# Performance work log

Hardware: AMD Instinct MI355X
Metric: run time of the kernel (lower is better)

## Reference

```python
import jax, jax.numpy as jnp
import numpy as np

V, E, H, T = 30000, 512, 512, 32
B, L = 64, 512


def setup_inputs() -> dict:
    key = jax.random.key(0)
    ks = jax.random.split(key, 14)
    n = lambda k, shape: (jax.random.normal(k, shape, jnp.float32) * 0.05)
    return {
        "x": jax.random.randint(ks[0], (B, L), 0, V),
        "embedding": n(ks[1], (V, E)),
        # PyTorch LSTM params, gate order (i, f, g, o); biases b_ih+b_hh fused
        "w_ih_f": n(ks[2], (4 * H, E)),
        "w_hh_f": n(ks[3], (4 * H, H)),
        "b_f": n(ks[4], (4 * H,)),
        "w_ih_b": n(ks[5], (4 * H, E)),
        "w_hh_b": n(ks[6], (4 * H, H)),
        "b_b": n(ks[7], (4 * H,)),
        "W": n(ks[8], (T, 2 * H)),
        "b": n(ks[9], (T,)),
        # CRF params (torchcrf)
        "start": n(ks[10], (T,)),
        "end": n(ks[11], (T,)),
        "trans": n(ks[12], (T, T)),
    }


def _lstm(x, w_ih, w_hh, bias):
    # x: [L, B, E] -> hidden states [L, B, H]; PyTorch gate equations
    h_dim = w_hh.shape[1]
    xp = jnp.einsum('lbe,ge->lbg', x, w_ih) + bias  # precompute input proj [L,B,4H]

    def step(carry, xt):
        h, c = carry
        g = xt + h @ w_hh.T
        i, f, gg, o = jnp.split(g, 4, axis=-1)
        c = jax.nn.sigmoid(f) * c + jax.nn.sigmoid(i) * jnp.tanh(gg)
        h = jax.nn.sigmoid(o) * jnp.tanh(c)
        return (h, c), h

    bsz = x.shape[1]
    init = (jnp.zeros((bsz, h_dim), x.dtype), jnp.zeros((bsz, h_dim), x.dtype))
    _, hs = jax.lax.scan(step, init, xp)
    return hs


def _emissions(x, embedding, w_ih_f, w_hh_f, b_f, w_ih_b, w_hh_b, b_b, W, b):
    emb = embedding[x]                      # [B, L, E]
    xt = jnp.transpose(emb, (1, 0, 2))      # [L, B, E]
    hf = _lstm(xt, w_ih_f, w_hh_f, b_f)     # [L, B, H]
    hb = _lstm(xt[::-1], w_ih_b, w_hh_b, b_b)[::-1]
    h = jnp.concatenate([hf, hb], axis=-1)  # [L, B, 2H]
    return h @ W.T + b                      # [L, B, T]


def _viterbi(em, start, end, trans):
    # em: [L, B, T]; torchcrf CRF.decode with no mask (all timesteps valid)
    score = start + em[0]                   # [B, T]

    def step(score, em_t):
        nxt = score[:, :, None] + trans[None] + em_t[:, None, :]  # [B, T_prev, T_cur]
        return jnp.max(nxt, axis=1), jnp.argmax(nxt, axis=1)

    score, hist = jax.lax.scan(step, score, em[1:])  # hist: [L-1, B, T]
    score = score + end
    last = jnp.argmax(score, axis=-1)       # [B]

    def back(tag, idx_t):
        prev = jnp.take_along_axis(idx_t, tag[:, None], axis=1)[:, 0]
        return prev, prev

    _, prevs = jax.lax.scan(back, last, hist, reverse=True)  # [L-1, B]
    tags = jnp.concatenate([prevs, last[None]], axis=0)      # [L, B]
    return tags.T.astype(jnp.int32)                          # [B, L]


def reference(x, embedding, w_ih_f, w_hh_f, b_f, w_ih_b, w_hh_b, b_b, W, b, start, end, trans):
    em = _emissions(x, embedding, w_ih_f, w_hh_f, b_f, w_ih_b, w_hh_b, b_b, W, b)
    return _viterbi(em, start, end, trans)
```

## Files before the change

### kernel.cpp

```cpp
#include <hip/hip_runtime.h>
#include <cstdio>
#include <cstdint>


typedef float f32x4 __attribute__((ext_vector_type(4)));
typedef float f32x2 __attribute__((ext_vector_type(2)));

#define PKFMA(ACC, W2, H2) \
    asm("v_pk_fma_f32 %0, %1, %2, %0" : "+v"(ACC) : "v"(W2), "v"(H2))

__global__ __launch_bounds__(512) void k_gather(
    const int* __restrict__ x, const float* __restrict__ emb,
    float4* __restrict__ eg4)
{
    const int t   = blockIdx.x;
    const int tid = threadIdx.x;
    __shared__ int xv[64];
    if (tid < 64) xv[tid] = x[tid * 512 + t];
    __syncthreads();
    #pragma unroll
    for (int i = 0; i < 16; ++i) {
        const int flat = i * 512 + tid;
        const int b  = flat & 63;
        const int e4 = flat >> 6;
        const float4 v = *reinterpret_cast<const float4*>(
            emb + (size_t)xv[b] * 512 + e4 * 4);
        eg4[((size_t)t * 128 + e4) * 64 + b] = v;
    }
}

__global__ __launch_bounds__(256) void k_pack(
    const float* __restrict__ wih_f, const float* __restrict__ whh_f,
    const float* __restrict__ wih_b, const float* __restrict__ whh_b,
    float* __restrict__ wpack)
{
    const int i = blockIdx.x * 256 + threadIdx.x;
    const int j   = i & 3;
    const int r   = (i >> 2) & 7;
    const int kc  = (i >> 5) & 15;
    const int sec = (i >> 9) & 1;
    const int ks  = (i >> 10) & 7;
    const int wg  = (i >> 13) & 255;
    const int dir = (i >> 21) & 1;
    const int k   = ks * 64 + kc * 4 + j;
    const int g   = r >> 1, colL = r & 1;
    const int rg  = g * 512 + wg * 2 + colL;
    const float* wih = dir ? wih_b : wih_f;
    const float* whh = dir ? whh_b : whh_f;
    const float v = sec ? whh[(size_t)rg * 512 + k] : wih[(size_t)rg * 512 + k];
    wpack[i] = v;
}

__global__ __launch_bounds__(512, 2) void k_lstm(
    const float4* __restrict__ eg4, const float* __restrict__ wpack,
    const float* __restrict__ b_f, const float* __restrict__ b_b,
    float* __restrict__ h_f, float* __restrict__ h_b,
    int* __restrict__ bar)
{
    const int bid = blockIdx.x;
    const int dir = bid >> 8;
    const int wg  = bid & 255;
    float* HH       = dir ? h_b : h_f;
    const float* BS = dir ? b_b : b_f;
    int* ctr = bar + (size_t)dir * 65536;

    const int tid = threadIdx.x;
    const int b   = tid & 63;
    const int ks  = __builtin_amdgcn_readfirstlane(tid >> 6);

    __shared__ float wlds[8][1024];
    __shared__ float partb[8 * 8 * 64];
    __shared__ float hlds[64][2];

    {
        const float4* src = reinterpret_cast<const float4*>(
            wpack + (size_t)((dir * 256 + wg) * 8 + ks) * 1024);
        float4* dst = reinterpret_cast<float4*>(&wlds[ks][0]);
        #pragma unroll
        for (int i = 0; i < 4; ++i)
            dst[i * 64 + b] = src[i * 64 + b];
    }

    const int colL = (tid >> 6) & 1;
    float bias4[4] = {0.f, 0.f, 0.f, 0.f};
    if (tid < 128) {
        #pragma unroll
        for (int g = 0; g < 4; ++g) bias4[g] = BS[g * 512 + wg * 2 + colL];
    }
    float cst = 0.f;
    __syncthreads();

    const float* wl = &wlds[ks][0];

    f32x2 eacc2[8];
    #pragma unroll
    for (int r = 0; r < 8; ++r) eacc2[r] = (f32x2){0.f, 0.f};

    {
        const int t0 = dir ? 511 : 0;
        const float4* ep = eg4 + ((size_t)t0 * 128 + ks * 16) * 64 + b;
        #pragma unroll
        for (int half = 0; half < 2; ++half) {
            f32x4 v[8];
            #pragma unroll
            for (int kc = 0; kc < 8; ++kc)
                v[kc] = *reinterpret_cast<const f32x4*>(ep + (size_t)(half * 8 + kc) * 64);
            #pragma unroll
            for (int kc = 0; kc < 8; ++kc) {
                const float* wp = wl + (half * 8 + kc) * 32;
                const f32x2 elo = __builtin_shufflevector(v[kc], v[kc], 0, 1);
                const f32x2 ehi = __builtin_shufflevector(v[kc], v[kc], 2, 3);
                #pragma unroll
                for (int r = 0; r < 8; ++r) {
                    const f32x4 w4 = *reinterpret_cast<const f32x4*>(wp + r * 4);
                    const f32x2 wlo = __builtin_shufflevector(w4, w4, 0, 1);
                    const f32x2 whi = __builtin_shufflevector(w4, w4, 2, 3);
                    PKFMA(eacc2[r], wlo, elo);
                    PKFMA(eacc2[r], whi, ehi);
                }
            }
        }
    }

    for (int s = 0; s < 512; ++s) {
        const int t = dir ? (511 - s) : s;
        f32x2 acc2[8];
        #pragma unroll
        for (int r = 0; r < 8; ++r) acc2[r] = eacc2[r];

        if (s > 0) {
            const int* fp = ctr + ((size_t)(s - 1) * 8 + ks) * 16;
            while (__hip_atomic_load(fp, __ATOMIC_RELAXED,
                                     __HIP_MEMORY_SCOPE_AGENT) < 32)
                __builtin_amdgcn_s_sleep(1);

            const int tp = dir ? (t + 1) : (t - 1);
            const f32x2* hq = reinterpret_cast<const f32x2*>(HH)
                              + ((size_t)tp * 256 + ks * 32) * 64 + b;
            #pragma unroll
            for (int half = 0; half < 2; ++half) {
                f32x2 hv[16];
                #pragma unroll
                for (int kq = 0; kq < 16; ++kq)
                    hv[kq] = hq[(size_t)(half * 16 + kq) * 64];
                #pragma unroll
                for (int kc = 0; kc < 8; ++kc) {
                    const float* wp = wl + 512 + (half * 8 + kc) * 32;
                    #pragma unroll
                    for (int r = 0; r < 8; ++r) {
                        const f32x4 w4 = *reinterpret_cast<const f32x4*>(wp + r * 4);
                        const f32x2 wlo = __builtin_shufflevector(w4, w4, 0, 1);
                        const f32x2 whi = __builtin_shufflevector(w4, w4, 2, 3);
                        PKFMA(acc2[r], wlo, hv[kc * 2]);
                        PKFMA(acc2[r], whi, hv[kc * 2 + 1]);
                    }
                }
            }
        }

        #pragma unroll
        for (int r = 0; r < 8; ++r)
            partb[(ks * 8 + r) * 64 + b] = acc2[r][0] + acc2[r][1];
        __syncthreads();

        if (tid < 128) {
            float g4[4];
            #pragma unroll
            for (int g = 0; g < 4; ++g) {
                const int r = g * 2 + colL;
                float v = bias4[g];
                #pragma unroll
                for (int w = 0; w < 8; ++w) v += partb[(w * 8 + r) * 64 + b];
                g4[g] = v;
            }
            const float si = 1.f / (1.f + expf(-g4[0]));
            const float sf = 1.f / (1.f + expf(-g4[1]));
            const float tg = tanhf(g4[2]);
            const float so = 1.f / (1.f + expf(-g4[3]));
            cst = sf * cst + si * tg;
            hlds[b][colL] = so * tanhf(cst);
        }
        __syncthreads();

        if (tid < 64) {
            f32x2 o;
            o[0] = hlds[tid][0]; o[1] = hlds[tid][1];
            float* dst = HH + (((size_t)t * 256 + wg) * 64 + tid) * 2;
            asm volatile("global_store_dwordx2 %0, %1, off sc1"
                         :: "v"(dst), "v"(o) : "memory");
            asm volatile("s_waitcnt vmcnt(0)" ::: "memory");
            if (tid == 0 && s < 511)
                __hip_atomic_fetch_add(
                    ctr + ((size_t)s * 8 + (wg >> 5)) * 16, 1,
                    __ATOMIC_RELAXED, __HIP_MEMORY_SCOPE_AGENT);
        }

        if (s < 511) {
            const int tn = dir ? (t - 1) : (t + 1);
            const float4* ep = eg4 + ((size_t)tn * 128 + ks * 16) * 64 + b;
            #pragma unroll
            for (int r = 0; r < 8; ++r) eacc2[r] = (f32x2){0.f, 0.f};
            #pragma unroll
            for (int half = 0; half < 2; ++half) {
                f32x4 v[8];
                #pragma unroll
                for (int kc = 0; kc < 8; ++kc)
                    v[kc] = *reinterpret_cast<const f32x4*>(ep + (size_t)(half * 8 + kc) * 64);
                #pragma unroll
                for (int kc = 0; kc < 8; ++kc) {
                    const float* wp = wl + (half * 8 + kc) * 32;
                    const f32x2 elo = __builtin_shufflevector(v[kc], v[kc], 0, 1);
                    const f32x2 ehi = __builtin_shufflevector(v[kc], v[kc], 2, 3);
                    #pragma unroll
                    for (int r = 0; r < 8; ++r) {
                        const f32x4 w4 = *reinterpret_cast<const f32x4*>(wp + r * 4);
                        const f32x2 wlo = __builtin_shufflevector(w4, w4, 0, 1);
                        const f32x2 whi = __builtin_shufflevector(w4, w4, 2, 3);
                        PKFMA(eacc2[r], wlo, elo);
                        PKFMA(eacc2[r], whi, ehi);
                    }
                }
            }
        }
    }
}

__global__ __launch_bounds__(256) void k_em(
    const float* __restrict__ hf, const float* __restrict__ hb,
    const float* __restrict__ Wm, const float* __restrict__ bias,
    float* __restrict__ em)
{
    const int t   = blockIdx.x;
    const int tid = threadIdx.x;
    const int b   = tid & 63;
    const int tg  = tid >> 6;
    __shared__ float Wl[128][33];
    float acc[8] = {};

    for (int ch = 0; ch < 8; ++ch) {
        {
            const int tag = tid >> 3;
            const int kq  = tid & 7;
            const float* src = Wm + (size_t)tag * 1024 + ch * 128 + kq * 16;
            #pragma unroll
            for (int ii = 0; ii < 4; ++ii) {
                const float4 v = *reinterpret_cast<const float4*>(src + ii * 4);
                const int k0 = kq * 16 + ii * 4;
                Wl[k0 + 0][tag] = v.x; Wl[k0 + 1][tag] = v.y;
                Wl[k0 + 2][tag] = v.z; Wl[k0 + 3][tag] = v.w;
            }
        }
        __syncthreads();
        const f32x2* hsrc2 = (ch < 4)
            ? (reinterpret_cast<const f32x2*>(hf) + ((size_t)t * 256 + ch * 64) * 64 + b)
            : (reinterpret_cast<const f32x2*>(hb) + ((size_t)t * 256 + (ch - 4) * 64) * 64 + b);
        #pragma unroll 4
        for (int c2l = 0; c2l < 64; ++c2l) {
            const f32x2 h2 = hsrc2[(size_t)c2l * 64];
            #pragma unroll
            for (int j = 0; j < 2; ++j)
                #pragma unroll
                for (int jt = 0; jt < 8; ++jt)
                    acc[jt] = fmaf(h2[j], Wl[c2l * 2 + j][tg * 8 + jt], acc[jt]);
        }
        __syncthreads();
    }

    #pragma unroll
    for (int jt = 0; jt < 8; ++jt) {
        const int tag = tg * 8 + jt;
        em[((size_t)t * 64 + b) * 32 + tag] = acc[jt] + bias[tag];
    }
}

__global__ __launch_bounds__(64) void k_vit(
    const float* __restrict__ em, const float* __restrict__ startv,
    const float* __restrict__ endv, const float* __restrict__ trans,
    int* __restrict__ out)
{
    const int b    = blockIdx.x;
    const int lane = threadIdx.x;
    const int c    = lane & 31;
    const bool act = lane < 32;
    __shared__ unsigned char hist[511][32];
    __shared__ int outb[512];

    float tr[32];
    #pragma unroll 8
    for (int p = 0; p < 32; ++p) tr[p] = trans[p * 32 + c];

    float s = act ? (startv[c] + em[(size_t)b * 32 + c]) : -1e30f;

    for (int t = 1; t < 512; ++t) {
        const float emc = act ? em[((size_t)t * 64 + b) * 32 + c] : 0.f;
        float m = -1e30f; int arg = 0;
        #pragma unroll 8
        for (int p = 0; p < 32; ++p) {
            const float v = __shfl(s, p) + tr[p] + emc;
            if (v > m) { m = v; arg = p; }
        }
        if (act) { s = m; hist[t - 1][c] = (unsigned char)arg; }
    }

    s = act ? (s + endv[c]) : -1e30f;
    int idx = act ? c : 63;
    #pragma unroll
    for (int off = 32; off >= 1; off >>= 1) {
        const float om = __shfl_down(s, off);
        const int   oi = __shfl_down(idx, off);
        if (om > s || (om == s && oi < idx)) { s = om; idx = oi; }
    }
    idx = __shfl(idx, 0);

    if (lane == 0) {
        int tag = idx;
        outb[511] = tag;
        for (int t = 510; t >= 0; --t) { tag = hist[t][tag]; outb[t] = tag; }
    }
    __syncthreads();
    for (int i = lane; i < 512; i += 64) out[(size_t)b * 512 + i] = outb[i];
}

extern "C" void kernel_launch(void* const* d_in, const int* in_sizes, int n_in,
                              void* d_out, int out_size, void* d_ws, size_t ws_size,
                              hipStream_t stream)
{
    const int*   x      = (const int*)d_in[0];
    const float* emb    = (const float*)d_in[1];
    const float* w_ih_f = (const float*)d_in[2];
    const float* w_hh_f = (const float*)d_in[3];
    const float* b_f    = (const float*)d_in[4];
    const float* w_ih_b = (const float*)d_in[5];
    const float* w_hh_b = (const float*)d_in[6];
    const float* b_b    = (const float*)d_in[7];
    const float* Wm     = (const float*)d_in[8];
    const float* bvec   = (const float*)d_in[9];
    const float* startv = (const float*)d_in[10];
    const float* endv   = (const float*)d_in[11];
    const float* trans  = (const float*)d_in[12];
    int* out = (int*)d_out;

    float* ws    = (float*)d_ws;
    float* eg    = ws;
    float* h_f   = ws + 16777216;
    float* h_b   = ws + 33554432;
    float* em    = ws + 50331648;
    float* wpack = ws + 51380224;
    int*   bar   = (int*)(ws + 55574528);

    const size_t need = (size_t)(55574528 + 131072) * 4;
    if (ws_size < need) {
        fprintf(stderr, "kernel_launch: ws too small: %zu < %zu\n", ws_size, need);
        return;
    }

    (void)hipMemsetAsync(bar, 0, 524288, stream);
    k_gather<<<dim3(512),   512, 0, stream>>>(x, emb, (float4*)eg);
    k_pack  <<<dim3(16384), 256, 0, stream>>>(w_ih_f, w_hh_f, w_ih_b, w_hh_b, wpack);
    k_lstm  <<<dim3(512),   512, 0, stream>>>((const float4*)eg, wpack, b_f, b_b,
                                              h_f, h_b, bar);
    k_em    <<<dim3(512),   256, 0, stream>>>(h_f, h_b, Wm, bvec, em);
    k_vit   <<<dim3(64),     64, 0, stream>>>(em, startv, endv, trans, out);
}
```

Baseline: 6.382 ms.

## Compute LSTM input projection with split-bf16 MFMA instead of packed FP32 FMA

The per-step input projection (W_ih · x_t) moves from v_pk_fma_f32 loops to MFMA 16x16x32 bf16. To keep accuracy, weights and embeddings are each split into a hi/lo bf16 pair and combined with three MFMAs. The gather kernel now emits embeddings directly in the MFMA B-fragment layout, and a new pack kernel builds the A fragments held in registers. Results are double-buffered in LDS and added during the gate reduction. This halves the weight LDS footprint and takes VALU work off the serial step loop, at the cost of a small precision loss, half-empty MFMA tiles (only 8 of 16 rows are used), and an extra pack launch.

Result: slower. 7.014 ms (+9.9%).

```diff
diff --git a/kernel.cpp b/kernel.cpp
--- a/kernel.cpp
+++ b/kernel.cpp
@@ -5,13 +5,20 @@
 
 typedef float f32x4 __attribute__((ext_vector_type(4)));
 typedef float f32x2 __attribute__((ext_vector_type(2)));
+typedef short bf16x8 __attribute__((ext_vector_type(8)));
+typedef unsigned short u16x4 __attribute__((ext_vector_type(4)));
 
 #define PKFMA(ACC, W2, H2) \
     asm("v_pk_fma_f32 %0, %1, %2, %0" : "+v"(ACC) : "v"(W2), "v"(H2))
 
+__device__ __forceinline__ unsigned short bf16_rne(float x) {
+    unsigned u = __float_as_uint(x);
+    return (unsigned short)((u + 0x7FFF + ((u >> 16) & 1)) >> 16);
+}
+
 __global__ __launch_bounds__(512) void k_gather(
     const int* __restrict__ x, const float* __restrict__ emb,
-    float4* __restrict__ eg4)
+    unsigned short* __restrict__ egf)
 {
     const int t   = blockIdx.x;
     const int tid = threadIdx.x;
@@ -20,12 +27,31 @@
     __syncthreads();
     #pragma unroll
     for (int i = 0; i < 16; ++i) {
-        const int flat = i * 512 + tid;
-        const int b  = flat & 63;
-        const int e4 = flat >> 6;
+        const int unit = i * 512 + tid;
+        const int b  = unit >> 7;
+        const int k0 = (unit & 127) * 4;
         const float4 v = *reinterpret_cast<const float4*>(
-            emb + (size_t)xv[b] * 512 + e4 * 4);
-        eg4[((size_t)t * 128 + e4) * 64 + b] = v;
+            emb + (size_t)xv[b] * 512 + k0);
+        const int ks   = k0 >> 6;
+        const int kt   = (k0 >> 5) & 1;
+        const int kk0  = k0 & 31;
+        const int lgrp = (kk0 >> 2) & 3;
+        const int rq   = kk0 >> 4;
+        const int l    = lgrp * 16 + (b & 15);
+        const int nt   = b >> 4;
+        const size_t base =
+            ((((((size_t)t * 8 + ks) * 2 + kt) * 4 + nt) * 2 + 0) * 64 + l) * 8 + rq * 4;
+        const float xs[4] = {v.x, v.y, v.z, v.w};
+        u16x4 hi, lo;
+        #pragma unroll
+        for (int j = 0; j < 4; ++j) {
+            const unsigned short h = bf16_rne(xs[j]);
+            hi[j] = h;
+            const float hf = __uint_as_float(((unsigned)h) << 16);
+            lo[j] = bf16_rne(xs[j] - hf);
+        }
+        *reinterpret_cast<u16x4*>(egf + base)       = hi;
+        *reinterpret_cast<u16x4*>(egf + base + 512) = lo;
     }
 }
 
@@ -51,8 +77,37 @@
     wpack[i] = v;
 }
 
+__global__ __launch_bounds__(256) void k_packA(
+    const float* __restrict__ wih_f, const float* __restrict__ wih_b,
+    unsigned short* __restrict__ afrag)
+{
+    const int idx = blockIdx.x * 256 + threadIdx.x;
+    const int r   = idx & 7;
+    const int l   = (idx >> 3) & 63;
+    const int sel = (idx >> 9) & 1;
+    const int kt  = (idx >> 10) & 1;
+    const int ks  = (idx >> 11) & 7;
+    const int wg  = (idx >> 14) & 255;
+    const int dir = (idx >> 22) & 1;
+    const int i   = l & 15;
+    float w = 0.f;
+    if (i < 8) {
+        const int rg = (i >> 1) * 512 + wg * 2 + (i & 1);
+        const int k  = ks * 64 + kt * 32 + (r >> 2) * 16 + ((l >> 4) & 3) * 4 + (r & 3);
+        w = (dir ? wih_b : wih_f)[(size_t)rg * 512 + k];
+    }
+    const unsigned short hi = bf16_rne(w);
+    unsigned short outv = hi;
+    if (sel) {
+        const float hf = __uint_as_float(((unsigned)hi) << 16);
+        outv = bf16_rne(w - hf);
+    }
+    afrag[idx] = outv;
+}
+
 __global__ __launch_bounds__(512, 2) void k_lstm(
-    const float4* __restrict__ eg4, const float* __restrict__ wpack,
+    const unsigned short* __restrict__ egf, const float* __restrict__ wpack,
+    const unsigned short* __restrict__ afrag,
     const float* __restrict__ b_f, const float* __restrict__ b_b,
     float* __restrict__ h_f, float* __restrict__ h_b,
     int* __restrict__ bar)
@@ -68,17 +123,29 @@
     const int b   = tid & 63;
     const int ks  = __builtin_amdgcn_readfirstlane(tid >> 6);
 
-    __shared__ float wlds[8][1024];
+    __shared__ float wlds[8][512];
     __shared__ float partb[8 * 8 * 64];
+    __shared__ float elds[2][8][8][64];
     __shared__ float hlds[64][2];
 
     {
         const float4* src = reinterpret_cast<const float4*>(
-            wpack + (size_t)((dir * 256 + wg) * 8 + ks) * 1024);
+            wpack + (size_t)((dir * 256 + wg) * 8 + ks) * 1024 + 512);
         float4* dst = reinterpret_cast<float4*>(&wlds[ks][0]);
         #pragma unroll
-        for (int i = 0; i < 4; ++i)
+        for (int i = 0; i < 2; ++i)
             dst[i * 64 + b] = src[i * 64 + b];
+    }
+
+    bf16x8 aHi[2], aLo[2];
+    {
+        const unsigned short* af = afrag
+            + (size_t)((dir * 256 + wg) * 8 + ks) * 2048;
+        #pragma unroll
+        for (int kt = 0; kt < 2; ++kt) {
+            aHi[kt] = *reinterpret_cast<const bf16x8*>(af + ((kt * 2 + 0) * 64 + b) * 8);
+            aLo[kt] = *reinterpret_cast<const bf16x8*>(af + ((kt * 2 + 1) * 64 + b) * 8);
+        }
     }
 
     const int colL = (tid >> 6) & 1;
@@ -88,45 +155,40 @@
         for (int g = 0; g < 4; ++g) bias4[g] = BS[g * 512 + wg * 2 + colL];
     }
     float cst = 0.f;
-    __syncthreads();
-
-    const float* wl = &wlds[ks][0];
-
-    f32x2 eacc2[8];
-    #pragma unroll
-    for (int r = 0; r < 8; ++r) eacc2[r] = (f32x2){0.f, 0.f};
 
     {
         const int t0 = dir ? 511 : 0;
-        const float4* ep = eg4 + ((size_t)t0 * 128 + ks * 16) * 64 + b;
-        #pragma unroll
-        for (int half = 0; half < 2; ++half) {
-            f32x4 v[8];
-            #pragma unroll
-            for (int kc = 0; kc < 8; ++kc)
-                v[kc] = *reinterpret_cast<const f32x4*>(ep + (size_t)(half * 8 + kc) * 64);
-            #pragma unroll
-            for (int kc = 0; kc < 8; ++kc) {
-                const float* wp = wl + (half * 8 + kc) * 32;
-                const f32x2 elo = __builtin_shufflevector(v[kc], v[kc], 0, 1);
-                const f32x2 ehi = __builtin_shufflevector(v[kc], v[kc], 2, 3);
-                #pragma unroll
-                for (int r = 0; r < 8; ++r) {
-                    const f32x4 w4 = *reinterpret_cast<const f32x4*>(wp + r * 4);
-                    const f32x2 wlo = __builtin_shufflevector(w4, w4, 0, 1);
-                    const f32x2 whi = __builtin_shufflevector(w4, w4, 2, 3);
-                    PKFMA(eacc2[r], wlo, elo);
-                    PKFMA(eacc2[r], whi, ehi);
-                }
-            }
-        }
-    }
+        const unsigned short* ef = egf + (size_t)t0 * 65536 + (size_t)ks * 8192;
+        #pragma unroll
+        for (int nt = 0; nt < 4; ++nt) {
+            f32x4 d = {0.f, 0.f, 0.f, 0.f};
+            #pragma unroll
+            for (int kt = 0; kt < 2; ++kt) {
+                const bf16x8 bh = *reinterpret_cast<const bf16x8*>(
+                    ef + (((kt * 4 + nt) * 2 + 0) * 64 + b) * 8);
+                const bf16x8 bl = *reinterpret_cast<const bf16x8*>(
+                    ef + (((kt * 4 + nt) * 2 + 1) * 64 + b) * 8);
+                d = __builtin_amdgcn_mfma_f32_16x16x32_bf16(aHi[kt], bh, d, 0, 0, 0);
+                d = __builtin_amdgcn_mfma_f32_16x16x32_bf16(aHi[kt], bl, d, 0, 0, 0);
+                d = __builtin_amdgcn_mfma_f32_16x16x32_bf16(aLo[kt], bh, d, 0, 0, 0);
+            }
+            const int i0 = (b >> 4) * 4;
+            if (i0 < 8) {
+                #pragma unroll
+                for (int g = 0; g < 4; ++g)
+                    elds[0][ks][i0 + g][nt * 16 + (b & 15)] = d[g];
+            }
+        }
+    }
+    __syncthreads();
+
+    const float* wl = &wlds[ks][0];
 
     for (int s = 0; s < 512; ++s) {
         const int t = dir ? (511 - s) : s;
         f32x2 acc2[8];
         #pragma unroll
-        for (int r = 0; r < 8; ++r) acc2[r] = eacc2[r];
+        for (int r = 0; r < 8; ++r) acc2[r] = (f32x2){0.f, 0.f};
 
         if (s > 0) {
             const int* fp = ctr + ((size_t)(s - 1) * 8 + ks) * 16;
@@ -145,7 +207,7 @@
                     hv[kq] = hq[(size_t)(half * 16 + kq) * 64];
                 #pragma unroll
                 for (int kc = 0; kc < 8; ++kc) {
-                    const float* wp = wl + 512 + (half * 8 + kc) * 32;
+                    const float* wp = wl + (half * 8 + kc) * 32;
                     #pragma unroll
                     for (int r = 0; r < 8; ++r) {
                         const f32x4 w4 = *reinterpret_cast<const f32x4*>(wp + r * 4);
@@ -171,6 +233,8 @@
                 float v = bias4[g];
                 #pragma unroll
                 for (int w = 0; w < 8; ++w) v += partb[(w * 8 + r) * 64 + b];
+                #pragma unroll
+                for (int w = 0; w < 8; ++w) v += elds[s & 1][w][r][b];
                 g4[g] = v;
             }
             const float si = 1.f / (1.f + expf(-g4[0]));
@@ -197,28 +261,25 @@
 
         if (s < 511) {
             const int tn = dir ? (t - 1) : (t + 1);
-            const float4* ep = eg4 + ((size_t)tn * 128 + ks * 16) * 64 + b;
-            #pragma unroll
-            for (int r = 0; r < 8; ++r) eacc2[r] = (f32x2){0.f, 0.f};
-            #pragma unroll
-            for (int half = 0; half < 2; ++half) {
-                f32x4 v[8];
-                #pragma unroll
-                for (int kc = 0; kc < 8; ++kc)
-                    v[kc] = *reinterpret_cast<const f32x4*>(ep + (size_t)(half * 8 + kc) * 64);
-                #pragma unroll
-                for (int kc = 0; kc < 8; ++kc) {
-                    const float* wp = wl + (half * 8 + kc) * 32;
-                    const f32x2 elo = __builtin_shufflevector(v[kc], v[kc], 0, 1);
-                    const f32x2 ehi = __builtin_shufflevector(v[kc], v[kc], 2, 3);
+            const unsigned short* ef = egf + (size_t)tn * 65536 + (size_t)ks * 8192;
+            #pragma unroll
+            for (int nt = 0; nt < 4; ++nt) {
+                f32x4 d = {0.f, 0.f, 0.f, 0.f};
+                #pragma unroll
+                for (int kt = 0; kt < 2; ++kt) {
+                    const bf16x8 bh = *reinterpret_cast<const bf16x8*>(
+                        ef + (((kt * 4 + nt) * 2 + 0) * 64 + b) * 8);
+                    const bf16x8 bl = *reinterpret_cast<const bf16x8*>(
+                        ef + (((kt * 4 + nt) * 2 + 1) * 64 + b) * 8);
+                    d = __builtin_amdgcn_mfma_f32_16x16x32_bf16(aHi[kt], bh, d, 0, 0, 0);
+                    d = __builtin_amdgcn_mfma_f32_16x16x32_bf16(aHi[kt], bl, d, 0, 0, 0);
+                    d = __builtin_amdgcn_mfma_f32_16x16x32_bf16(aLo[kt], bh, d, 0, 0, 0);
+                }
+                const int i0 = (b >> 4) * 4;
+                if (i0 < 8) {
                     #pragma unroll
-                    for (int r = 0; r < 8; ++r) {
-                        const f32x4 w4 = *reinterpret_cast<const f32x4*>(wp + r * 4);
-                        const f32x2 wlo = __builtin_shufflevector(w4, w4, 0, 1);
-                        const f32x2 whi = __builtin_shufflevector(w4, w4, 2, 3);
-                        PKFMA(eacc2[r], wlo, elo);
-                        PKFMA(eacc2[r], whi, ehi);
-                    }
+                    for (int g = 0; g < 4; ++g)
+                        elds[(s + 1) & 1][ks][i0 + g][nt * 16 + (b & 15)] = d[g];
                 }
             }
         }
@@ -340,24 +401,26 @@
     const float* trans  = (const float*)d_in[12];
     int* out = (int*)d_out;
 
-    float* ws    = (float*)d_ws;
-    float* eg    = ws;
+    float* ws = (float*)d_ws;
+    unsigned short* egf = (unsigned short*)ws;
     float* h_f   = ws + 16777216;
     float* h_b   = ws + 33554432;
     float* em    = ws + 50331648;
     float* wpack = ws + 51380224;
-    int*   bar   = (int*)(ws + 55574528);
-
-    const size_t need = (size_t)(55574528 + 131072) * 4;
+    unsigned short* afrag = (unsigned short*)(ws + 55574528);
+    int*   bar   = (int*)(ws + 59768832);
+
+    const size_t need = (size_t)(59768832 + 131072) * 4;
     if (ws_size < need) {
         fprintf(stderr, "kernel_launch: ws too small: %zu < %zu\n", ws_size, need);
         return;
     }
 
     (void)hipMemsetAsync(bar, 0, 524288, stream);
-    k_gather<<<dim3(512),   512, 0, stream>>>(x, emb, (float4*)eg);
+    k_gather<<<dim3(512),   512, 0, stream>>>(x, emb, egf);
     k_pack  <<<dim3(16384), 256, 0, stream>>>(w_ih_f, w_hh_f, w_ih_b, w_hh_b, wpack);
-    k_lstm  <<<dim3(512),   512, 0, stream>>>((const float4*)eg, wpack, b_f, b_b,
+    k_packA <<<dim3(32768), 256, 0, stream>>>(w_ih_f, w_ih_b, afrag);
+    k_lstm  <<<dim3(512),   512, 0, stream>>>(egf, wpack, afrag, b_f, b_b,
                                               h_f, h_b, bar);
     k_em    <<<dim3(512),   256, 0, stream>>>(h_f, h_b, Wm, bvec, em);
     k_vit   <<<dim3(64),     64, 0, stream>>>(em, startv, endv, trans, out);
```
